# Performance work log

Measured on AMD Instinct MI355X. Metric: run time of the kernel, lower is better.

Reference implementation:

```python
import jax, jax.numpy as jnp
import numpy as np

D_MODEL = 1024
D_STATE = 16
D_CONV = 4
EXPAND = 2
D_INNER = EXPAND * D_MODEL          # 2048
DT_RANK = D_MODEL // 16             # 64 (ceil(d_model/16))
BATCH = 4
SEQ = 2048


def setup_inputs() -> dict:
    key = jax.random.key(0)
    ks = jax.random.split(key, 9)
    s = lambda k, shape, sc: jax.random.normal(k, shape, jnp.float32) * sc
    x = s(ks[0], (BATCH, SEQ, D_MODEL), 1.0)
    W_in = s(ks[1], (2 * D_INNER, D_MODEL), D_MODEL ** -0.5)       # in_proj (no bias)
    conv_w = s(ks[2], (D_INNER, D_CONV), D_CONV ** -0.5)           # depthwise causal conv1d
    conv_b = s(ks[3], (D_INNER,), 0.02)
    W_xproj = s(ks[4], (DT_RANK + 2 * D_STATE, D_INNER), D_INNER ** -0.5)  # x_proj (no bias)
    W_dt = s(ks[5], (D_INNER, DT_RANK), DT_RANK ** -0.5)           # dt_proj weight
    b_dt = jax.random.uniform(ks[6], (D_INNER,), jnp.float32, -4.0, -1.0)  # dt_proj bias (small dt init)
    # S4D-real init: A_log = log([1..d_state]) per channel
    A_log = jnp.log(jnp.tile(jnp.arange(1, D_STATE + 1, dtype=jnp.float32), (D_INNER, 1)))
    D_skip = jnp.ones((D_INNER,), jnp.float32)
    W_out = s(ks[7], (D_MODEL, D_INNER), D_INNER ** -0.5)          # out_proj (no bias)
    return dict(x=x, W_in=W_in, conv_w=conv_w, conv_b=conv_b, W_xproj=W_xproj,
                W_dt=W_dt, b_dt=b_dt, A_log=A_log, D_skip=D_skip, W_out=W_out)


def reference(x, W_in, conv_w, conv_b, W_xproj, W_dt, b_dt, A_log, D_skip, W_out):
    silu = jax.nn.silu
    # in_proj -> split into x stream and gate z
    xz = jnp.einsum('bld,ed->ble', x, W_in)              # (B, L, 2*d_inner)
    xi, z = jnp.split(xz, 2, axis=-1)
    # causal depthwise conv1d (pad left d_conv-1), small fixed K loop
    K = conv_w.shape[1]
    L = xi.shape[1]
    xpad = jnp.pad(xi, ((0, 0), (K - 1, 0), (0, 0)))
    xc = sum(xpad[:, k:k + L, :] * conv_w[:, k] for k in range(K))
    u = silu(xc + conv_b)                                # (B, L, d_inner)
    # x_proj -> dt, B, C
    dbl = jnp.einsum('blc,ec->ble', u, W_xproj)          # (B, L, dt_rank + 2*d_state)
    dt = jax.nn.softplus(jnp.einsum('blr,cr->blc', dbl[..., :DT_RANK], W_dt) + b_dt)  # (B,L,d_inner)
    Bs = dbl[..., DT_RANK:DT_RANK + D_STATE]             # (B, L, d_state)
    Cs = dbl[..., DT_RANK + D_STATE:]                    # (B, L, d_state)
    A = -jnp.exp(A_log)                                  # (d_inner, d_state)

    # selective scan: h_t = exp(dt_t * A) * h_{t-1} + dt_t * B_t * u_t ; y_t = <h_t, C_t>
    def step(h, inp):
        dt_t, B_t, C_t, u_t = inp                        # (B,d_inner),(B,ds),(B,ds),(B,d_inner)
        dA = jnp.exp(dt_t[:, :, None] * A)               # (B, d_inner, d_state)
        h = h * dA + (dt_t * u_t)[:, :, None] * B_t[:, None, :]
        y = jnp.einsum('bcs,bs->bc', h, C_t)
        return h, y

    h0 = jnp.zeros((x.shape[0], D_INNER, D_STATE), x.dtype)
    xs = (jnp.swapaxes(dt, 0, 1), jnp.swapaxes(Bs, 0, 1),
          jnp.swapaxes(Cs, 0, 1), jnp.swapaxes(u, 0, 1))
    _, ys = jax.lax.scan(step, h0, xs)                   # ys: (L, B, d_inner)
    y = jnp.swapaxes(ys, 0, 1) + u * D_skip              # skip connection D*u
    y = y * silu(z)                                      # gate
    return jnp.einsum('blc,dc->bld', y, W_out)           # out_proj -> (B, L, d_model)
```

## Files before the change

### kernel.cpp

```cpp
#include <hip/hip_runtime.h>

#define AS1 __attribute__((address_space(1)))
#define AS3 __attribute__((address_space(3)))

typedef unsigned short ushort_t;
typedef __attribute__((ext_vector_type(8))) short short8;
typedef __attribute__((ext_vector_type(4))) float floatx4;

__device__ __forceinline__ float bf2f(ushort_t h) {
    return __uint_as_float(((unsigned int)h) << 16);
}
__device__ __forceinline__ ushort_t f2bf(float f) {
    unsigned int u = __float_as_uint(f);
    u += 0x7fffu + ((u >> 16) & 1u);
    return (ushort_t)(u >> 16);
}

__global__ __launch_bounds__(256) void cast_all(
    const float* __restrict__ s0, ushort_t* __restrict__ d0,
    const float* __restrict__ s1, ushort_t* __restrict__ d1,
    const float* __restrict__ s2, ushort_t* __restrict__ d2,
    const float* __restrict__ s3, ushort_t* __restrict__ d3,
    const float* __restrict__ s4, ushort_t* __restrict__ d4)
{
    int i = blockIdx.x * 256 + threadIdx.x;
    const float* src; ushort_t* dst; int off;
    if      (i < 2097152) { src = s0; dst = d0; off = i; }
    else if (i < 3145728) { src = s1; dst = d1; off = i - 2097152; }
    else if (i < 3194880) { src = s2; dst = d2; off = i - 3145728; }
    else if (i < 3227648) { src = s3; dst = d3; off = i - 3194880; }
    else                  { src = s4; dst = d4; off = i - 3227648; }
    float4 v = ((const float4*)src)[off];
    ((ushort4*)dst)[off] = make_ushort4(f2bf(v.x), f2bf(v.y), f2bf(v.z), f2bf(v.w));
}

template <int MODE>
__global__ __launch_bounds__(512, 2) void gemm8p(
    const ushort_t* __restrict__ A, int lda,
    const ushort_t* __restrict__ B, int ldb,
    int K, ushort_t* __restrict__ outH, ushort_t* __restrict__ outH2,
    int Mtiles, int Ntiles)
{
    __shared__ ushort_t sA[2][16384];
    __shared__ ushort_t sB[2][16384];

    const int tid = threadIdx.x;

    const int xcd = blockIdx.x & 7;
    const int k8  = blockIdx.x >> 3;
    const int m0  = (((xcd >> 1) << 3) + (k8 >> 3)) * 256;
    const int n0  = (((xcd & 1) << 3) + (k8 & 7)) * 256;

    const int lane = tid & 63, wave = tid >> 6;
    const int wm = (wave >> 2) * 128, wn = (wave & 3) * 64;
    const int lm = lane & 15, quad = lane >> 4, lm7 = lane & 7;

    const int r0 = tid >> 3;
    const int hh = (tid & 7) ^ (r0 & 7);
    const ushort_t* pA = A + (size_t)(m0 + r0) * lda + hh * 8;
    const ushort_t* pB = B + (size_t)(n0 + r0) * ldb + hh * 8;

#define STG_A(buf, tt, rowoff)                                                        \
    __builtin_amdgcn_global_load_lds(                                                 \
        (const AS1 void*)(pA + (size_t)(rowoff) * lda + (tt) * 64),                   \
        (AS3 void*)(&sA[buf][(rowoff) * 64 + tid * 8]), 16, 0, 0)
#define STG_B(buf, tt, rowoff)                                                        \
    __builtin_amdgcn_global_load_lds(                                                 \
        (const AS1 void*)(pB + (size_t)(rowoff) * ldb + (tt) * 64),                   \
        (AS3 void*)(&sB[buf][(rowoff) * 64 + tid * 8]), 16, 0, 0)
#define SLOT0(buf, tt) { STG_A(buf, tt, 0);   STG_A(buf, tt, 64);  }
#define SLOT1(buf, tt) { STG_A(buf, tt, 128); STG_A(buf, tt, 192); }
#define SLOT2(buf, tt) { STG_B(buf, tt, 0);   STG_B(buf, tt, 64);  }
#define SLOT3(buf, tt) { STG_B(buf, tt, 128); STG_B(buf, tt, 192); }

#define BARRIER() asm volatile("s_barrier" ::: "memory")

#define LD_A(buf, h)                                                                  \
    { _Pragma("unroll")                                                               \
      for (int ii = 0; ii < 4; ++ii) {                                                \
          int row = wm + (h) * 64 + ii * 16 + lm;                                     \
          a_[ii][0] = *(const short8*)&sA[buf][(row * 8 + (quad ^ lm7)) * 8];         \
          a_[ii][1] = *(const short8*)&sA[buf][(row * 8 + ((4 + quad) ^ lm7)) * 8];   \
      } }
#define LD_B2(buf, j0)                                                                \
    { _Pragma("unroll")                                                               \
      for (int jj = 0; jj < 2; ++jj) {                                                \
          int row = wn + ((j0) + jj) * 16 + lm;                                       \
          b_[(j0) + jj][0] = *(const short8*)&sB[buf][(row * 8 + (quad ^ lm7)) * 8];  \
          b_[(j0) + jj][1] = *(const short8*)&sB[buf][(row * 8 + ((4 + quad) ^ lm7)) * 8]; \
      } }
#define MFMA16(i0, j0)                                                                \
    { __builtin_amdgcn_s_setprio(1);                                                  \
      _Pragma("unroll")                                                               \
      for (int ii = 0; ii < 4; ++ii) {                                                \
          _Pragma("unroll")                                                           \
          for (int jj = 0; jj < 2; ++jj) {                                            \
              acc[(i0) + ii][(j0) + jj] = __builtin_amdgcn_mfma_f32_16x16x32_bf16(    \
                  a_[ii][0], b_[(j0) + jj][0], acc[(i0) + ii][(j0) + jj], 0, 0, 0);   \
              acc[(i0) + ii][(j0) + jj] = __builtin_amdgcn_mfma_f32_16x16x32_bf16(    \
                  a_[ii][1], b_[(j0) + jj][1], acc[(i0) + ii][(j0) + jj], 0, 0, 0);   \
          } }                                                                         \
      __builtin_amdgcn_s_setprio(0); }

    floatx4 acc[8][4];
#pragma unroll
    for (int i = 0; i < 8; ++i)
#pragma unroll
        for (int j = 0; j < 4; ++j)
            acc[i][j] = (floatx4){0.f, 0.f, 0.f, 0.f};

    short8 a_[4][2], b_[4][2];
    const int NT = K >> 6;

    SLOT0(0, 0); SLOT1(0, 0); SLOT2(0, 0); SLOT3(0, 0);
    SLOT0(1, 1);
    asm volatile("s_waitcnt vmcnt(2)" ::: "memory");
    BARRIER();

    for (int t = 0; t < NT; ++t) {
        const int p = t & 1, q = p ^ 1;
        LD_A(p, 0);
        LD_B2(p, 0);
        if (t + 1 < NT) { SLOT1(q, t + 1); SLOT2(q, t + 1); }
        MFMA16(0, 0);
        LD_B2(p, 2);
        if (t + 1 < NT) { SLOT3(q, t + 1); }
        MFMA16(0, 2);
        LD_A(p, 1);
        MFMA16(4, 2);
        BARRIER();
        if (t + 2 < NT) SLOT0(p, t + 2);
        MFMA16(4, 0);
        if (t + 2 < NT) { asm volatile("s_waitcnt vmcnt(2)" ::: "memory"); }
        else            { asm volatile("s_waitcnt vmcnt(0)" ::: "memory"); }
        BARRIER();
    }

#pragma unroll
    for (int idx = 0; idx < 8; ++idx) {
        const int rowb = m0 + wm + (idx >> 2) * 64 + (idx & 3) * 16 + quad * 4;
#pragma unroll
        for (int j = 0; j < 4; ++j) {
            const int col = n0 + wn + j * 16 + lm;
#pragma unroll
            for (int r = 0; r < 4; ++r) {
                float v = acc[idx][j][r];
                const size_t rr = (size_t)(rowb + r);
                if (MODE == 0) {
                    if (col < 2048) outH[rr * 2048 + col] = f2bf(v);
                    else            outH2[rr * 2048 + (col - 2048)] = f2bf(v);
                }
            }
        }
    }
#undef STG_A
#undef STG_B
#undef SLOT0
#undef SLOT1
#undef SLOT2
#undef SLOT3
#undef BARRIER
#undef LD_A
#undef LD_B2
#undef MFMA16
}

template <int MODE>
__global__ __launch_bounds__(256) void gemm_bt(
    const ushort_t* __restrict__ A, int lda,
    const ushort_t* __restrict__ B, int ldb,
    int K, int Nact, int ldc,
    float* __restrict__ outF, ushort_t* __restrict__ outH,
    ushort_t* __restrict__ outH2, const float* __restrict__ biasF)
{
    constexpr int BM = 128, BN = 128, BK = 64;
    __shared__ ushort_t sA[BM * BK];
    __shared__ ushort_t sB[BN * BK];
    const int tid  = threadIdx.x;
    const int m0   = blockIdx.x * BM;
    const int seg  = (MODE == 4) ? blockIdx.y : 0;
    const int n0   = (MODE == 4) ? 0 : blockIdx.y * BN;
    if (MODE == 4) { A += seg * 512; B += seg * 512; }
    const int lane = tid & 63, wave = tid >> 6;
    const int wm   = (wave & 1) * 64, wn = (wave >> 1) * 64;
    const int lm   = lane & 15, quad = lane >> 4;
    const int lm7  = lane & 7;

    floatx4 acc[4][4];
#pragma unroll
    for (int i = 0; i < 4; ++i)
#pragma unroll
        for (int j = 0; j < 4; ++j)
            acc[i][j] = (floatx4){0.f, 0.f, 0.f, 0.f};

    for (int k0 = 0; k0 < K; k0 += BK) {
        __syncthreads();
#pragma unroll
        for (int r = 0; r < 4; ++r) {
            int g   = r * 256 + tid;
            int row = g >> 3;
            int hh  = (g & 7) ^ (row & 7);
            int col = k0 + hh * 8;
            const ushort_t* gA = A + (size_t)(m0 + row) * lda + col;
            __builtin_amdgcn_global_load_lds((const AS1 void*)gA, (AS3 void*)(&sA[g * 8]), 16, 0, 0);
            int rowB = n0 + row;
            if (rowB >= Nact) rowB = Nact - 1;
            const ushort_t* gB = B + (size_t)rowB * ldb + col;
            __builtin_amdgcn_global_load_lds((const AS1 void*)gB, (AS3 void*)(&sB[g * 8]), 16, 0, 0);
        }
        __syncthreads();

#pragma unroll
        for (int s = 0; s < 2; ++s) {
            short8 af[4], bfr[4];
#pragma unroll
            for (int i = 0; i < 4; ++i) {
                int row = wm + i * 16 + lm;
                int gr  = row * 8 + ((s * 4 + quad) ^ lm7);
                af[i] = *(const short8*)&sA[gr * 8];
            }
#pragma unroll
            for (int j = 0; j < 4; ++j) {
                int row = wn + j * 16 + lm;
                int gr  = row * 8 + ((s * 4 + quad) ^ lm7);
                bfr[j] = *(const short8*)&sB[gr * 8];
            }
#pragma unroll
            for (int i = 0; i < 4; ++i)
#pragma unroll
                for (int j = 0; j < 4; ++j)
                    acc[i][j] = __builtin_amdgcn_mfma_f32_16x16x32_bf16(af[i], bfr[j], acc[i][j], 0, 0, 0);
        }
    }

#pragma unroll
    for (int i = 0; i < 4; ++i) {
#pragma unroll
        for (int j = 0; j < 4; ++j) {
#pragma unroll
            for (int r = 0; r < 4; ++r) {
                int row = m0 + wm + i * 16 + quad * 4 + r;
                int col = n0 + wn + j * 16 + lm;
                float v = acc[i][j][r];
                if (MODE == 2) {
                    float x  = v + biasF[col];
                    float sp = (x > 20.f) ? x : log1pf(__expf(x));
                    _Float16 hv = (_Float16)sp;
                    outH[(size_t)row * ldc + col] = *(ushort_t*)&hv;
                } else if (MODE == 3) {
                    if (col < Nact) outF[(size_t)row * ldc + col] = v;
                } else if (MODE == 4) {
                    if (col < 96)
                        outF[(size_t)seg * 786432 + (size_t)row * 96 + col] = v;
                }
            }
        }
    }
}

__global__ __launch_bounds__(256) void comb3(
    const float* __restrict__ Pg, ushort_t* __restrict__ dbl,
    float* __restrict__ BCf)
{
    int i = blockIdx.x * 256 + threadIdx.x;
    float v = Pg[i] + Pg[i + 786432] + Pg[i + 2 * 786432] + Pg[i + 3 * 786432];
    dbl[i] = f2bf(v);
    int col = i % 96;
    if (col >= 64) BCf[(size_t)(i / 96) * 32 + (col - 64)] = v;
}

__global__ __launch_bounds__(256) void conv_silu_k(
    const ushort_t* __restrict__ xi, const float* __restrict__ conv_w,
    const float* __restrict__ conv_b, ushort_t* __restrict__ u)
{
    int idx = blockIdx.x * 256 + threadIdx.x;
    int c   = idx & 2047;
    int lg  = idx >> 11;
    int b   = lg >> 9;
    int l0  = (lg & 511) * 4;
    const size_t base = ((size_t)b * 2048 + l0) * 2048 + c;

    float w0 = conv_w[c * 4], w1 = conv_w[c * 4 + 1],
          w2 = conv_w[c * 4 + 2], w3 = conv_w[c * 4 + 3];
    float bias = conv_b[c];

    float xv[7];
#pragma unroll
    for (int j = 0; j < 3; ++j)
        xv[j] = (l0 - 3 + j >= 0) ? bf2f(xi[base + (j - 3) * 2048]) : 0.f;
#pragma unroll
    for (int j = 3; j < 7; ++j)
        xv[j] = bf2f(xi[base + (j - 3) * 2048]);

#pragma unroll
    for (int i = 0; i < 4; ++i) {
        float acc = bias + w0 * xv[i] + w1 * xv[i + 1] + w2 * xv[i + 2] + w3 * xv[i + 3];
        float s = acc / (1.f + __expf(-acc));
        u[base + i * 2048] = f2bf(s);
    }
}

constexpr int CH  = 64;
constexpr int NCH = 32;
constexpr int NI  = 4 * 2048 * 16;

__global__ __launch_bounds__(256) void scan_p1(
    const _Float16* __restrict__ dt, const ushort_t* __restrict__ u,
    const float* __restrict__ BC, const float* __restrict__ A_log,
    float* __restrict__ Pbuf, float* __restrict__ Sbuf)
{
    const int tid   = threadIdx.x;
    const int blk   = blockIdx.x;
    const int chunk = blk >> 5;
    const int b     = (blk >> 3) & 3;
    const int c     = ((blk & 7) << 8) + tid;
    const size_t base = (size_t)b * 2048 + chunk * CH;

    float As[16];
#pragma unroll
    for (int s = 0; s < 16; ++s) As[s] = -__expf(A_log[c * 16 + s]);

    float S[16];
#pragma unroll
    for (int s = 0; s < 16; ++s) S[s] = 0.f;
    float cumdt = 0.f;

    for (int t = 0; t < CH; ++t) {
        const size_t r = base + t;
        float dtv = (float)dt[r * 2048 + c];
        float uv  = bf2f(u[r * 2048 + c]);
        float ct  = dtv * uv;
        cumdt += dtv;
#pragma unroll
        for (int s = 0; s < 16; ++s) {
            float a = __expf(dtv * As[s]);
            S[s] = fmaf(S[s], a, ct * BC[r * 32 + s]);
        }
    }
    const size_t ob = (size_t)chunk * NI + (size_t)b * 2048 + c;
#pragma unroll
    for (int s = 0; s < 16; ++s) {
        Pbuf[ob + (size_t)s * 8192] = __expf(As[s] * cumdt);
        Sbuf[ob + (size_t)s * 8192] = S[s];
    }
}

__global__ __launch_bounds__(256) void scan_comb(
    const float* __restrict__ Pbuf, const float* __restrict__ Sbuf,
    float* __restrict__ Hbuf)
{
    const int i = blockIdx.x * 256 + threadIdx.x;
    float hi = 0.f;
#pragma unroll
    for (int k = 0; k < NCH; ++k) {
        Hbuf[(size_t)k * NI + i] = hi;
        hi = Sbuf[(size_t)k * NI + i] + Pbuf[(size_t)k * NI + i] * hi;
    }
}

__global__ __launch_bounds__(256) void scan_p2(
    const _Float16* __restrict__ dt, const ushort_t* __restrict__ u,
    const float* __restrict__ BC, const float* __restrict__ A_log,
    const float* __restrict__ D_skip, const float* __restrict__ Hbuf,
    ushort_t* __restrict__ zy)
{
    const int tid   = threadIdx.x;
    const int blk   = blockIdx.x;
    const int chunk = blk >> 5;
    const int b     = (blk >> 3) & 3;
    const int c     = ((blk & 7) << 8) + tid;
    const size_t base = (size_t)b * 2048 + chunk * CH;

    float As[16], h[16];
#pragma unroll
    for (int s = 0; s < 16; ++s) As[s] = -__expf(A_log[c * 16 + s]);
    const float Dsk = D_skip[c];
    const size_t ob = (size_t)chunk * NI + (size_t)b * 2048 + c;
#pragma unroll
    for (int s = 0; s < 16; ++s) h[s] = Hbuf[ob + (size_t)s * 8192];

    for (int t = 0; t < CH; ++t) {
        const size_t r = base + t;
        float dtv = (float)dt[r * 2048 + c];
        float uv  = bf2f(u[r * 2048 + c]);
        float zv  = bf2f(zy[r * 2048 + c]);
        float ct  = dtv * uv;
        float p0 = 0.f, p1 = 0.f, p2 = 0.f, p3 = 0.f;
#pragma unroll
        for (int s = 0; s < 16; s += 4) {
            float a0 = __expf(dtv * As[s]);
            float a1 = __expf(dtv * As[s + 1]);
            float a2 = __expf(dtv * As[s + 2]);
            float a3 = __expf(dtv * As[s + 3]);
            h[s]     = fmaf(h[s],     a0, ct * BC[r * 32 + s]);
            h[s + 1] = fmaf(h[s + 1], a1, ct * BC[r * 32 + s + 1]);
            h[s + 2] = fmaf(h[s + 2], a2, ct * BC[r * 32 + s + 2]);
            h[s + 3] = fmaf(h[s + 3], a3, ct * BC[r * 32 + s + 3]);
            p0 = fmaf(h[s],     BC[r * 32 + 16 + s],     p0);
            p1 = fmaf(h[s + 1], BC[r * 32 + 16 + s + 1], p1);
            p2 = fmaf(h[s + 2], BC[r * 32 + 16 + s + 2], p2);
            p3 = fmaf(h[s + 3], BC[r * 32 + 16 + s + 3], p3);
        }
        float p = (p0 + p1) + (p2 + p3);
        float g = zv / (1.f + __expf(-zv));
        float yv = (p + uv * Dsk) * g;
        zy[r * 2048 + c] = f2bf(yv);
    }
}

extern "C" void kernel_launch(void* const* d_in, const int* in_sizes, int n_in,
                              void* d_out, int out_size, void* d_ws, size_t ws_size,
                              hipStream_t stream)
{
    const float* x      = (const float*)d_in[0];
    const float* W_in   = (const float*)d_in[1];
    const float* conv_w = (const float*)d_in[2];
    const float* conv_b = (const float*)d_in[3];
    const float* W_xp   = (const float*)d_in[4];
    const float* W_dt   = (const float*)d_in[5];
    const float* b_dt   = (const float*)d_in[6];
    const float* A_log  = (const float*)d_in[7];
    const float* D_skip = (const float*)d_in[8];
    const float* W_out  = (const float*)d_in[9];

    char* ws = (char*)d_ws;
    const size_t MB = 1024 * 1024;
    ushort_t*  xi  = (ushort_t*)(ws);
    ushort_t*  xw  = (ushort_t*)(ws + 32 * MB);
    ushort_t*  Wib = (ushort_t*)(ws + 48 * MB);
    _Float16*  dt  = (_Float16*)(ws);
    float*     Pg  = (float*)(ws + 32 * MB);
    float*     Pb  = (float*)(ws + 32 * MB);
    float*     Sb  = (float*)(ws + 48 * MB);
    ushort_t*  z   = (ushort_t*)(ws + 64 * MB);
    ushort_t*  u   = (ushort_t*)(ws + 96 * MB);
    ushort_t*  dbl = (ushort_t*)(ws + 128 * MB);
    ushort_t*  Wxb = (ushort_t*)(ws + 130 * MB);
    ushort_t*  Wdb = (ushort_t*)(ws + 131 * MB);
    ushort_t*  Wob = (ushort_t*)(ws + 132 * MB);
    float*     BCf = (float*)(ws + 137 * MB);
    float*     Hb  = (float*)(ws + 138 * MB);

    cast_all<<<14656, 256, 0, stream>>>(x, xw, W_in, Wib, W_xp, Wxb, W_dt, Wdb, W_out, Wob);

    gemm8p<0><<<512, 512, 0, stream>>>(xw, 1024, Wib, 1024, 1024, xi, z, 32, 16);
    conv_silu_k<<<16384, 256, 0, stream>>>(xi, conv_w, conv_b, u);
    gemm_bt<4><<<dim3(64, 4), 256, 0, stream>>>(u, 2048, Wxb, 2048, 512, 96, 96,
                                                Pg, nullptr, nullptr, nullptr);
    comb3<<<3072, 256, 0, stream>>>(Pg, dbl, BCf);
    gemm_bt<2><<<dim3(64, 16), 256, 0, stream>>>(dbl, 96, Wdb, 64, 64, 2048, 2048,
                                                 nullptr, (ushort_t*)dt, nullptr, b_dt);
    scan_p1<<<1024, 256, 0, stream>>>(dt, u, BCf, A_log, Pb, Sb);
    scan_comb<<<512, 256, 0, stream>>>(Pb, Sb, Hb);
    scan_p2<<<1024, 256, 0, stream>>>(dt, u, BCf, A_log, D_skip, Hb, z);
    gemm_bt<3><<<dim3(64, 8), 256, 0, stream>>>(z, 2048, Wob, 2048, 2048, 1024, 1024,
                                                (float*)d_out, nullptr, nullptr, nullptr);
}
```

Before: 460.3 us.

## Fuse causal depthwise conv and SiLU into in_proj GEMM epilogue

The in_proj GEMM epilogue now computes the causal depthwise conv plus SiLU directly from accumulator registers. It uses wave shuffles to get the previous rows inside each 128-row wave tile, so the xi intermediate is no longer written and read back by a separate conv kernel. The first three rows of each wave tile need rows held by another tile, so the boundary values go to a small buffer and a tiny conv_fix kernel finishes those rows. This also adds an lgkmcnt wait before a barrier in the main loop and a heavier epilogue, which may raise register pressure.

```diff
diff --git a/kernel.cpp b/kernel.cpp
--- a/kernel.cpp
+++ b/kernel.cpp
@@ -14,6 +14,9 @@
     unsigned int u = __float_as_uint(f);
     u += 0x7fffu + ((u >> 16) & 1u);
     return (ushort_t)(u >> 16);
+}
+__device__ __forceinline__ float silu_f(float a) {
+    return a / (1.f + __expf(-a));
 }
 
 __global__ __launch_bounds__(256) void cast_all(
@@ -34,12 +37,12 @@
     ((ushort4*)dst)[off] = make_ushort4(f2bf(v.x), f2bf(v.y), f2bf(v.z), f2bf(v.w));
 }
 
-template <int MODE>
-__global__ __launch_bounds__(512, 2) void gemm8p(
+__global__ __launch_bounds__(512, 2) void gemm1_fused(
     const ushort_t* __restrict__ A, int lda,
     const ushort_t* __restrict__ B, int ldb,
-    int K, ushort_t* __restrict__ outH, ushort_t* __restrict__ outH2,
-    int Mtiles, int Ntiles)
+    int K, ushort_t* __restrict__ outU, ushort_t* __restrict__ outZ,
+    const float* __restrict__ conv_w, const float* __restrict__ conv_b,
+    ushort_t* __restrict__ Bxi)
 {
     __shared__ ushort_t sA[2][16384];
     __shared__ ushort_t sB[2][16384];
@@ -128,6 +131,7 @@
         MFMA16(0, 2);
         LD_A(p, 1);
         MFMA16(4, 2);
+        asm volatile("s_waitcnt lgkmcnt(0)" ::: "memory");
         BARRIER();
         if (t + 2 < NT) SLOT0(p, t + 2);
         MFMA16(4, 0);
@@ -136,20 +140,60 @@
         BARRIER();
     }
 
-#pragma unroll
-    for (int idx = 0; idx < 8; ++idx) {
-        const int rowb = m0 + wm + (idx >> 2) * 64 + (idx & 3) * 16 + quad * 4;
+    if (n0 >= 2048) {
+#pragma unroll
+        for (int idx = 0; idx < 8; ++idx) {
+            const int rowb = m0 + wm + (idx >> 2) * 64 + (idx & 3) * 16 + quad * 4;
+#pragma unroll
+            for (int j = 0; j < 4; ++j) {
+                const int col = n0 + wn + j * 16 + lm - 2048;
+#pragma unroll
+                for (int r = 0; r < 4; ++r)
+                    outZ[(size_t)(rowb + r) * 2048 + col] = f2bf(acc[idx][j][r]);
+            }
+        }
+    } else {
+        const int wt   = (m0 + wm) >> 7;
+        const int srcl = (lane - 16) & 63;
 #pragma unroll
         for (int j = 0; j < 4; ++j) {
             const int col = n0 + wn + j * 16 + lm;
-#pragma unroll
-            for (int r = 0; r < 4; ++r) {
-                float v = acc[idx][j][r];
-                const size_t rr = (size_t)(rowb + r);
-                if (MODE == 0) {
-                    if (col < 2048) outH[rr * 2048 + col] = f2bf(v);
-                    else            outH2[rr * 2048 + (col - 2048)] = f2bf(v);
+            const float4 wv = *(const float4*)&conv_w[col * 4];
+            const float bias = conv_b[col];
+            float c1 = 0.f, c2 = 0.f, c3 = 0.f;
+#pragma unroll
+            for (int g8 = 0; g8 < 8; ++g8) {
+                const float x0 = acc[g8][j][0], x1 = acc[g8][j][1],
+                            x2 = acc[g8][j][2], x3 = acc[g8][j][3];
+                const float s1 = (quad == 3) ? c3 : x3;
+                const float s2 = (quad == 3) ? c2 : x2;
+                const float s3 = (quad == 3) ? c1 : x1;
+                const float m1 = __shfl(s1, srcl, 64);
+                const float m2 = __shfl(s2, srcl, 64);
+                const float m3 = __shfl(s3, srcl, 64);
+                float u0 = bias + wv.x * m3 + wv.y * m2 + wv.z * m1 + wv.w * x0;
+                float u1 = bias + wv.x * m2 + wv.y * m1 + wv.z * x0 + wv.w * x1;
+                float u2 = bias + wv.x * m1 + wv.y * x0 + wv.z * x1 + wv.w * x2;
+                float u3 = bias + wv.x * x0 + wv.y * x1 + wv.z * x2 + wv.w * x3;
+                const int row0 = m0 + wm + (g8 >> 2) * 64 + (g8 & 3) * 16 + quad * 4;
+                const bool first = (g8 == 0) && (quad == 0);
+                if (!first) {
+                    outU[(size_t)(row0 + 0) * 2048 + col] = f2bf(silu_f(u0));
+                    outU[(size_t)(row0 + 1) * 2048 + col] = f2bf(silu_f(u1));
+                    outU[(size_t)(row0 + 2) * 2048 + col] = f2bf(silu_f(u2));
                 }
+                outU[(size_t)(row0 + 3) * 2048 + col] = f2bf(silu_f(u3));
+                if (first) {
+                    Bxi[((size_t)wt * 6 + 0) * 2048 + col] = f2bf(x0);
+                    Bxi[((size_t)wt * 6 + 1) * 2048 + col] = f2bf(x1);
+                    Bxi[((size_t)wt * 6 + 2) * 2048 + col] = f2bf(x2);
+                }
+                if (g8 == 7 && quad == 3) {
+                    Bxi[((size_t)wt * 6 + 3) * 2048 + col] = f2bf(x1);
+                    Bxi[((size_t)wt * 6 + 4) * 2048 + col] = f2bf(x2);
+                    Bxi[((size_t)wt * 6 + 5) * 2048 + col] = f2bf(x3);
+                }
+                c1 = x1; c2 = x2; c3 = x3;
             }
         }
     }
@@ -163,6 +207,33 @@
 #undef LD_A
 #undef LD_B2
 #undef MFMA16
+}
+
+__global__ __launch_bounds__(256) void conv_fix(
+    const ushort_t* __restrict__ Bxi, const float* __restrict__ conv_w,
+    const float* __restrict__ conv_b, ushort_t* __restrict__ u)
+{
+    int i  = blockIdx.x * 256 + threadIdx.x;
+    int c  = i & 2047;
+    int wt = i >> 11;
+    int m0w = wt << 7;
+    float p0 = 0.f, p1 = 0.f, p2 = 0.f;
+    if ((m0w & 2047) != 0) {
+        p0 = bf2f(Bxi[((size_t)(wt - 1) * 6 + 3) * 2048 + c]);
+        p1 = bf2f(Bxi[((size_t)(wt - 1) * 6 + 4) * 2048 + c]);
+        p2 = bf2f(Bxi[((size_t)(wt - 1) * 6 + 5) * 2048 + c]);
+    }
+    float x0 = bf2f(Bxi[((size_t)wt * 6 + 0) * 2048 + c]);
+    float x1 = bf2f(Bxi[((size_t)wt * 6 + 1) * 2048 + c]);
+    float x2 = bf2f(Bxi[((size_t)wt * 6 + 2) * 2048 + c]);
+    const float4 wv = *(const float4*)&conv_w[c * 4];
+    const float bias = conv_b[c];
+    float u0 = bias + wv.x * p0 + wv.y * p1 + wv.z * p2 + wv.w * x0;
+    float u1 = bias + wv.x * p1 + wv.y * p2 + wv.z * x0 + wv.w * x1;
+    float u2 = bias + wv.x * p2 + wv.y * x0 + wv.z * x1 + wv.w * x2;
+    u[(size_t)(m0w + 0) * 2048 + c] = f2bf(silu_f(u0));
+    u[(size_t)(m0w + 1) * 2048 + c] = f2bf(silu_f(u1));
+    u[(size_t)(m0w + 2) * 2048 + c] = f2bf(silu_f(u2));
 }
 
 template <int MODE>
@@ -269,37 +340,6 @@
     if (col >= 64) BCf[(size_t)(i / 96) * 32 + (col - 64)] = v;
 }
 
-__global__ __launch_bounds__(256) void conv_silu_k(
-    const ushort_t* __restrict__ xi, const float* __restrict__ conv_w,
-    const float* __restrict__ conv_b, ushort_t* __restrict__ u)
-{
-    int idx = blockIdx.x * 256 + threadIdx.x;
-    int c   = idx & 2047;
-    int lg  = idx >> 11;
-    int b   = lg >> 9;
-    int l0  = (lg & 511) * 4;
-    const size_t base = ((size_t)b * 2048 + l0) * 2048 + c;
-
-    float w0 = conv_w[c * 4], w1 = conv_w[c * 4 + 1],
-          w2 = conv_w[c * 4 + 2], w3 = conv_w[c * 4 + 3];
-    float bias = conv_b[c];
-
-    float xv[7];
-#pragma unroll
-    for (int j = 0; j < 3; ++j)
-        xv[j] = (l0 - 3 + j >= 0) ? bf2f(xi[base + (j - 3) * 2048]) : 0.f;
-#pragma unroll
-    for (int j = 3; j < 7; ++j)
-        xv[j] = bf2f(xi[base + (j - 3) * 2048]);
-
-#pragma unroll
-    for (int i = 0; i < 4; ++i) {
-        float acc = bias + w0 * xv[i] + w1 * xv[i + 1] + w2 * xv[i + 2] + w3 * xv[i + 3];
-        float s = acc / (1.f + __expf(-acc));
-        u[base + i * 2048] = f2bf(s);
-    }
-}
-
 constexpr int CH  = 64;
 constexpr int NCH = 32;
 constexpr int NI  = 4 * 2048 * 16;
@@ -425,9 +465,9 @@
 
     char* ws = (char*)d_ws;
     const size_t MB = 1024 * 1024;
-    ushort_t*  xi  = (ushort_t*)(ws);
     ushort_t*  xw  = (ushort_t*)(ws + 32 * MB);
     ushort_t*  Wib = (ushort_t*)(ws + 48 * MB);
+    ushort_t*  Bxi = (ushort_t*)(ws + 56 * MB);
     _Float16*  dt  = (_Float16*)(ws);
     float*     Pg  = (float*)(ws + 32 * MB);
     float*     Pb  = (float*)(ws + 32 * MB);
@@ -443,8 +483,9 @@
 
     cast_all<<<14656, 256, 0, stream>>>(x, xw, W_in, Wib, W_xp, Wxb, W_dt, Wdb, W_out, Wob);
 
-    gemm8p<0><<<512, 512, 0, stream>>>(xw, 1024, Wib, 1024, 1024, xi, z, 32, 16);
-    conv_silu_k<<<16384, 256, 0, stream>>>(xi, conv_w, conv_b, u);
+    gemm1_fused<<<512, 512, 0, stream>>>(xw, 1024, Wib, 1024, 1024, u, z,
+                                         conv_w, conv_b, Bxi);
+    conv_fix<<<512, 256, 0, stream>>>(Bxi, conv_w, conv_b, u);
     gemm_bt<4><<<dim3(64, 4), 256, 0, stream>>>(u, 2048, Wxb, 2048, 512, 96, 96,
                                                 Pg, nullptr, nullptr, nullptr);
     comb3<<<3072, 256, 0, stream>>>(Pg, dbl, BCf);
```

New measurement: 459.9 us. About the same (-0.1%).
